# Kernel tuning notes

Hardware: AMD Instinct MI355X
Metric: run time of the kernel (lower is better)

The kernel has to match this reference:

```python
import jax, jax.numpy as jnp
import numpy as np


def setup_inputs() -> dict:
    key = jax.random.key(0)
    k1, k2 = jax.random.split(key)
    B, C, F, H, W = 2, 19, 4, 256, 384
    inp = jax.random.uniform(k1, (B, C, F, H, W), dtype=jnp.float32)
    target = jax.random.randint(k2, (B, F, H, W), 0, C, dtype=jnp.int64)
    return {"input": inp, "target": target}


def reference(input, target):
    """Multi-class Lovasz-Softmax loss, vectorized over classes.

    input:  [B, C, F, H, W] class probabilities in [0, 1]
    target: [B, F, H, W] integer labels in [0, C)
    (No ignore_index values present in the generated inputs, so the
    valid-pixel filter of the original is a no-op.)
    """
    B, C, F, H, W = input.shape
    # flatten to [N, C] pixels-by-classes, matching permute(0,2,3,4,1).view(-1,C)
    probs = jnp.transpose(input, (0, 2, 3, 4, 1)).reshape(-1, C)
    labels = target.reshape(-1)  # [N]

    fg = (labels[:, None] == jnp.arange(C)[None, :]).astype(probs.dtype)  # [N, C]
    errors = jnp.abs(fg - probs)  # [N, C]

    # descending sort per class column (one batched sort instead of C kernels)
    perm = jnp.argsort(-errors, axis=0)  # [N, C]
    errors_sorted = jnp.take_along_axis(errors, perm, axis=0)
    fg_sorted = jnp.take_along_axis(fg, perm, axis=0)

    # Lovasz gradient (Alg. 1), per class
    gts = jnp.sum(fg, axis=0)  # [C]
    intersection = gts[None, :] - jnp.cumsum(fg_sorted, axis=0)
    union = gts[None, :] + jnp.cumsum(1.0 - fg_sorted, axis=0)
    jaccard = 1.0 - intersection / union
    grad = jnp.concatenate([jaccard[:1], jaccard[1:] - jaccard[:-1]], axis=0)

    per_class_loss = jnp.sum(errors_sorted * grad, axis=0)  # [C]

    # mean over classes that are present (fg.sum() > 0), like the loop's `continue`
    present = gts > 0
    n_present = jnp.maximum(jnp.sum(present.astype(probs.dtype)), 1.0)
    return jnp.sum(jnp.where(present, per_class_loss, 0.0)) / n_present
```

## Files before the change

kernel.cpp:

```cpp
#include <hip/hip_runtime.h>
#include <hip/hip_bf16.h>


#define NCLS   19
#define FHW    393216
#define NPIX   786432
#define NB     2048
#define PIXPB  8192
#define NCHUNK (NPIX / PIXPB)
#define BPT    (NB / 256)

#define GH_WORDS (NCLS * NB)
#define LAB_OFF  (GH_WORDS * 4)
#define CL_OFF   (LAB_OFF + NPIX)

__device__ __forceinline__ void accum_one(unsigned int* h, float p, int lab, int c) {
    bool fg = (lab == c);
    float e = fg ? (1.0f - p) : p;
    unsigned int bits = __float_as_uint(1.0f + e);
    unsigned int bkt = (bits - 0x3F800000u) >> 12;
    bkt = min(bkt, (unsigned int)(NB - 1));
    atomicAdd(&h[bkt], 1u + (fg ? (1u << 20) : 0u));
}

__global__ __launch_bounds__(256) void prep_kernel(
        const int4* __restrict__ tgt4, uchar4* __restrict__ lab4,
        unsigned int* __restrict__ gH) {
    const int i = blockIdx.x * 256 + threadIdx.x;
    int4 l = tgt4[i];
    lab4[i] = make_uchar4((unsigned char)l.x, (unsigned char)l.y,
                          (unsigned char)l.z, (unsigned char)l.w);
    if (i < GH_WORDS) gH[i] = 0u;
}

__global__ __launch_bounds__(256) void hist_kernel(
        const float* __restrict__ input, const unsigned char* __restrict__ lab,
        unsigned int* __restrict__ gH) {
    __shared__ unsigned int h[NB];
    const int tid = threadIdx.x;
    const int c = blockIdx.y;
    const int chunk = blockIdx.x;

    #pragma unroll
    for (int i = tid; i < NB; i += 256) h[i] = 0u;
    __syncthreads();

    const int pix0 = chunk * PIXPB;
    const int b = pix0 / FHW;
    const int fhw0 = pix0 % FHW;
    const float4* __restrict__ p4 =
        (const float4*)(input + ((long long)(b * NCLS + c)) * FHW + fhw0);
    const uchar4* __restrict__ l4 = (const uchar4*)(lab + pix0);

    #pragma unroll
    for (int i = tid; i < PIXPB / 4; i += 256) {
        float4 p = p4[i];
        uchar4 l = l4[i];
        accum_one(h, p.x, l.x, c);
        accum_one(h, p.y, l.y, c);
        accum_one(h, p.z, l.z, c);
        accum_one(h, p.w, l.w, c);
    }
    __syncthreads();

    unsigned int* __restrict__ g = gH + c * NB;
    #pragma unroll
    for (int i = tid; i < NB; i += 256) {
        unsigned int v = h[i];
        if (v) atomicAdd(&g[i], v);
    }
}

__global__ __launch_bounds__(256) void scan_kernel(
        const unsigned int* __restrict__ gH,
        float* __restrict__ classLoss, unsigned int* __restrict__ Gtot) {
    const int c = blockIdx.x;
    const int tid = threadIdx.x;
    const unsigned int* __restrict__ g = gH + c * NB;

    unsigned int w[BPT];
    const int base = NB - BPT * (tid + 1);
    unsigned int sumN = 0, sumG = 0;
    #pragma unroll
    for (int j = 0; j < BPT; ++j) {
        w[j] = g[base + j];
        sumN += w[j] & 0xFFFFFu;
        sumG += w[j] >> 20;
    }

    __shared__ unsigned long long sd[256];
    const unsigned long long mine = ((unsigned long long)sumG << 32) | sumN;
    sd[tid] = mine;
    __syncthreads();
    for (int off = 1; off < 256; off <<= 1) {
        unsigned long long add = (tid >= off) ? sd[tid - off] : 0ull;
        __syncthreads();
        sd[tid] += add;
        __syncthreads();
    }
    const unsigned long long incl = sd[tid];
    const unsigned long long tot = sd[255];
    const unsigned long long exc = incl - mine;
    const unsigned int G = (unsigned int)(tot >> 32);

    if (G == 0) { if (tid == 0) { classLoss[c] = 0.0f; Gtot[c] = 0u; } return; }

    const float Gf = (float)G;
    unsigned int r = (unsigned int)exc;
    unsigned int cf = (unsigned int)(exc >> 32);
    float acc = 0.0f;
    #pragma unroll
    for (int j = BPT - 1; j >= 0; --j) {
        const unsigned int nb = w[j] & 0xFFFFFu;
        const unsigned int gb = w[j] >> 20;
        if (nb) {
            const float r0 = (float)r,          c0 = (float)cf;
            const float r1 = (float)(r + nb),   c1 = (float)(cf + gb);
            const float J0 = 1.0f - (Gf - c0) / (Gf + r0 - c0);
            const float J1 = 1.0f - (Gf - c1) / (Gf + r1 - c1);
            const float center = ((float)(base + j) + 0.5f) * (1.0f / (float)NB);
            acc += center * (J1 - J0);
        }
        r += nb; cf += gb;
    }

    __shared__ float sf[256];
    sf[tid] = acc;
    __syncthreads();
    for (int off = 128; off > 0; off >>= 1) {
        if (tid < off) sf[tid] += sf[tid + off];
        __syncthreads();
    }
    if (tid == 0) { classLoss[c] = sf[0]; Gtot[c] = G; }
}

__global__ void finalize_kernel(const unsigned int* __restrict__ Gtot,
                                const float* __restrict__ classLoss,
                                float* __restrict__ out) {
    if (threadIdx.x == 0 && blockIdx.x == 0) {
        float s = 0.0f; int cnt = 0;
        for (int c = 0; c < NCLS; ++c) {
            if (Gtot[c] > 0u) { s += classLoss[c]; ++cnt; }
        }
        out[0] = s / fmaxf((float)cnt, 1.0f);
    }
}

extern "C" void kernel_launch(void* const* d_in, const int* in_sizes, int n_in,
                              void* d_out, int out_size, void* d_ws, size_t ws_size,
                              hipStream_t stream) {
    const float* input = (const float*)d_in[0];
    const int* target = (const int*)d_in[1];
    float* out = (float*)d_out;

    unsigned int* gH = (unsigned int*)d_ws;
    unsigned char* lab = (unsigned char*)d_ws + LAB_OFF;
    float* classLoss = (float*)((unsigned char*)d_ws + CL_OFF);
    unsigned int* Gtot = (unsigned int*)(classLoss + NCLS);

    prep_kernel<<<NPIX / 4 / 256, 256, 0, stream>>>(
        (const int4*)target, (uchar4*)lab, gH);
    hist_kernel<<<dim3(NCHUNK, NCLS), 256, 0, stream>>>(input, lab, gH);
    scan_kernel<<<NCLS, 256, 0, stream>>>(gH, classLoss, Gtot);
    finalize_kernel<<<1, 64, 0, stream>>>(Gtot, classLoss, out);
}
```

Before: 102.9 us.

## Replace global histogram atomics with per-chunk partials and merge, drop prep/finalize

After: 112.7 us. +9.5%, slower.

```diff
diff --git a/kernel.cpp b/kernel.cpp
--- a/kernel.cpp
+++ b/kernel.cpp
@@ -1,5 +1,4 @@
 #include <hip/hip_runtime.h>
-#include <hip/hip_bf16.h>
 
 
 #define NCLS   19
@@ -11,35 +10,24 @@
 #define BPT    (NB / 256)
 
 #define GH_WORDS (NCLS * NB)
-#define LAB_OFF  (GH_WORDS * 4)
-#define CL_OFF   (LAB_OFF + NPIX)
+#define PH_WORDS (NCHUNK * GH_WORDS)
 
 __device__ __forceinline__ void accum_one(unsigned int* h, float p, int lab, int c) {
-    bool fg = (lab == c);
-    float e = fg ? (1.0f - p) : p;
+    const bool fg = (lab == c);
+    const float e = fg ? (1.0f - p) : p;
     unsigned int bits = __float_as_uint(1.0f + e);
     unsigned int bkt = (bits - 0x3F800000u) >> 12;
     bkt = min(bkt, (unsigned int)(NB - 1));
-    atomicAdd(&h[bkt], 1u + (fg ? (1u << 20) : 0u));
-}
-
-__global__ __launch_bounds__(256) void prep_kernel(
-        const int4* __restrict__ tgt4, uchar4* __restrict__ lab4,
-        unsigned int* __restrict__ gH) {
-    const int i = blockIdx.x * 256 + threadIdx.x;
-    int4 l = tgt4[i];
-    lab4[i] = make_uchar4((unsigned char)l.x, (unsigned char)l.y,
-                          (unsigned char)l.z, (unsigned char)l.w);
-    if (i < GH_WORDS) gH[i] = 0u;
+    atomicAdd(&h[bkt], 1u + ((unsigned int)fg << 20));
 }
 
 __global__ __launch_bounds__(256) void hist_kernel(
-        const float* __restrict__ input, const unsigned char* __restrict__ lab,
-        unsigned int* __restrict__ gH) {
+        const float* __restrict__ input, const int* __restrict__ target,
+        unsigned int* __restrict__ pH) {
     __shared__ unsigned int h[NB];
     const int tid = threadIdx.x;
+    const int chunk = blockIdx.x;
     const int c = blockIdx.y;
-    const int chunk = blockIdx.x;
 
     #pragma unroll
     for (int i = tid; i < NB; i += 256) h[i] = 0u;
@@ -50,12 +38,12 @@
     const int fhw0 = pix0 % FHW;
     const float4* __restrict__ p4 =
         (const float4*)(input + ((long long)(b * NCLS + c)) * FHW + fhw0);
-    const uchar4* __restrict__ l4 = (const uchar4*)(lab + pix0);
+    const int4* __restrict__ l4 = (const int4*)(target + pix0);
 
     #pragma unroll
     for (int i = tid; i < PIXPB / 4; i += 256) {
         float4 p = p4[i];
-        uchar4 l = l4[i];
+        int4 l = l4[i];
         accum_one(h, p.x, l.x, c);
         accum_one(h, p.y, l.y, c);
         accum_one(h, p.z, l.z, c);
@@ -63,17 +51,32 @@
     }
     __syncthreads();
 
-    unsigned int* __restrict__ g = gH + c * NB;
+    uint4* __restrict__ g4 = (uint4*)(pH + ((size_t)(chunk * NCLS + c)) * NB);
+    const uint4* __restrict__ h4 = (const uint4*)h;
     #pragma unroll
-    for (int i = tid; i < NB; i += 256) {
-        unsigned int v = h[i];
-        if (v) atomicAdd(&g[i], v);
+    for (int i = tid; i < NB / 4; i += 256) g4[i] = h4[i];
+}
+
+__global__ __launch_bounds__(256) void merge_kernel(
+        const unsigned int* __restrict__ pH, unsigned int* __restrict__ gH,
+        unsigned int* __restrict__ acc) {
+    const int d = blockIdx.x * 256 + threadIdx.x;
+    if (blockIdx.x == 0 && threadIdx.x < 4) acc[threadIdx.x] = 0u;
+    if (d >= GH_WORDS) return;
+    unsigned int s0 = 0, s1 = 0, s2 = 0, s3 = 0;
+    #pragma unroll
+    for (int k = 0; k < NCHUNK; k += 4) {
+        s0 += pH[(size_t)(k + 0) * GH_WORDS + d];
+        s1 += pH[(size_t)(k + 1) * GH_WORDS + d];
+        s2 += pH[(size_t)(k + 2) * GH_WORDS + d];
+        s3 += pH[(size_t)(k + 3) * GH_WORDS + d];
     }
+    gH[d] = (s0 + s1) + (s2 + s3);
 }
 
 __global__ __launch_bounds__(256) void scan_kernel(
-        const unsigned int* __restrict__ gH,
-        float* __restrict__ classLoss, unsigned int* __restrict__ Gtot) {
+        const unsigned int* __restrict__ gH, unsigned int* __restrict__ acc,
+        float* __restrict__ out) {
     const int c = blockIdx.x;
     const int tid = threadIdx.x;
     const unsigned int* __restrict__ g = gH + c * NB;
@@ -103,46 +106,45 @@
     const unsigned long long exc = incl - mine;
     const unsigned int G = (unsigned int)(tot >> 32);
 
-    if (G == 0) { if (tid == 0) { classLoss[c] = 0.0f; Gtot[c] = 0u; } return; }
-
-    const float Gf = (float)G;
-    unsigned int r = (unsigned int)exc;
-    unsigned int cf = (unsigned int)(exc >> 32);
-    float acc = 0.0f;
-    #pragma unroll
-    for (int j = BPT - 1; j >= 0; --j) {
-        const unsigned int nb = w[j] & 0xFFFFFu;
-        const unsigned int gb = w[j] >> 20;
-        if (nb) {
-            const float r0 = (float)r,          c0 = (float)cf;
-            const float r1 = (float)(r + nb),   c1 = (float)(cf + gb);
-            const float J0 = 1.0f - (Gf - c0) / (Gf + r0 - c0);
-            const float J1 = 1.0f - (Gf - c1) / (Gf + r1 - c1);
-            const float center = ((float)(base + j) + 0.5f) * (1.0f / (float)NB);
-            acc += center * (J1 - J0);
+    float accv = 0.0f;
+    if (G != 0u) {
+        const float Gf = (float)G;
+        unsigned int r = (unsigned int)exc;
+        unsigned int cf = (unsigned int)(exc >> 32);
+        float Jprev = __fdividef((float)r, Gf + (float)r - (float)cf);
+        #pragma unroll
+        for (int j = BPT - 1; j >= 0; --j) {
+            const unsigned int nb = w[j] & 0xFFFFFu;
+            const unsigned int gb = w[j] >> 20;
+            r += nb; cf += gb;
+            if (nb) {
+                const float Jnew = __fdividef((float)r, Gf + (float)r - (float)cf);
+                const float center = ((float)(base + j) + 0.5f) * (1.0f / (float)NB);
+                accv += center * (Jnew - Jprev);
+                Jprev = Jnew;
+            }
         }
-        r += nb; cf += gb;
     }
 
     __shared__ float sf[256];
-    sf[tid] = acc;
+    sf[tid] = accv;
     __syncthreads();
     for (int off = 128; off > 0; off >>= 1) {
         if (tid < off) sf[tid] += sf[tid + off];
         __syncthreads();
     }
-    if (tid == 0) { classLoss[c] = sf[0]; Gtot[c] = G; }
-}
-
-__global__ void finalize_kernel(const unsigned int* __restrict__ Gtot,
-                                const float* __restrict__ classLoss,
-                                float* __restrict__ out) {
-    if (threadIdx.x == 0 && blockIdx.x == 0) {
-        float s = 0.0f; int cnt = 0;
-        for (int c = 0; c < NCLS; ++c) {
-            if (Gtot[c] > 0u) { s += classLoss[c]; ++cnt; }
+    if (tid == 0) {
+        if (G != 0u) {
+            atomicAdd((float*)&acc[0], sf[0]);
+            atomicAdd(&acc[1], 1u);
         }
-        out[0] = s / fmaxf((float)cnt, 1.0f);
+        __threadfence();
+        const unsigned int t = atomicAdd(&acc[2], 1u);
+        if (t == NCLS - 1) {
+            const float s = atomicAdd((float*)&acc[0], 0.0f);
+            const unsigned int k = atomicAdd(&acc[1], 0u);
+            out[0] = s / fmaxf((float)k, 1.0f);
+        }
     }
 }
 
@@ -153,14 +155,12 @@
     const int* target = (const int*)d_in[1];
     float* out = (float*)d_out;
 
-    unsigned int* gH = (unsigned int*)d_ws;
-    unsigned char* lab = (unsigned char*)d_ws + LAB_OFF;
-    float* classLoss = (float*)((unsigned char*)d_ws + CL_OFF);
-    unsigned int* Gtot = (unsigned int*)(classLoss + NCLS);
+    unsigned int* ws = (unsigned int*)d_ws;
+    unsigned int* pH = ws;
+    unsigned int* gH = ws + PH_WORDS;
+    unsigned int* acc = gH + GH_WORDS;
 
-    prep_kernel<<<NPIX / 4 / 256, 256, 0, stream>>>(
-        (const int4*)target, (uchar4*)lab, gH);
-    hist_kernel<<<dim3(NCHUNK, NCLS), 256, 0, stream>>>(input, lab, gH);
-    scan_kernel<<<NCLS, 256, 0, stream>>>(gH, classLoss, Gtot);
-    finalize_kernel<<<1, 64, 0, stream>>>(Gtot, classLoss, out);
+    hist_kernel<<<dim3(NCHUNK, NCLS), 256, 0, stream>>>(input, target, pH);
+    merge_kernel<<<(GH_WORDS + 255) / 256, 256, 0, stream>>>(pH, gH, acc);
+    scan_kernel<<<NCLS, 256, 0, stream>>>(gH, acc, out);
 }
```
